# Kernel optimization log

Hardware: AMD Instinct MI355X
Metric: run time of the kernel (lower is better)

The kernel has to match this reference:

```python
import jax, jax.numpy as jnp
import numpy as np

NUM_SLOTS = 7
DIM = 4096
NUM_HEADS = 8
HEAD_DIM = DIM // NUM_HEADS
LN_EPS = 1e-5


def setup_inputs() -> dict:
    key = jax.random.key(0)
    ks = jax.random.split(key, 9)
    B, N = 8, 2048
    x = jax.random.normal(ks[0], (B, N, DIM), dtype=jnp.float32)
    slots = 1e-4 * jax.random.normal(ks[1], (NUM_SLOTS, DIM), dtype=jnp.float32)
    ln_g = jnp.ones((DIM,), jnp.float32)
    ln_b = jnp.zeros((DIM,), jnp.float32)
    # nn.MultiheadAttention packed in-projection: rows [Wq; Wk; Wv], each (DIM, DIM)
    s = 1.0 / np.sqrt(DIM)
    in_proj_w = jax.random.uniform(ks[2], (3 * DIM, DIM), jnp.float32, -s, s)
    in_proj_b = jnp.zeros((3 * DIM,), jnp.float32)
    out_proj_w = jax.random.uniform(ks[3], (DIM, DIM), jnp.float32, -s, s)
    out_proj_b = jnp.zeros((DIM,), jnp.float32)
    alpha = 0.1 * jax.random.normal(ks[4], (1,), jnp.float32)  # nonzero so gate path is active
    return {"x": x, "slots": slots, "ln_g": ln_g, "ln_b": ln_b,
            "in_proj_w": in_proj_w, "in_proj_b": in_proj_b,
            "out_proj_w": out_proj_w, "out_proj_b": out_proj_b, "alpha": alpha}


def _cmrm(x, slots, ln_g, ln_b, in_proj_w, in_proj_b, out_proj_w, out_proj_b, alpha):
    x32 = x.astype(jnp.float32)
    # pre LayerNorm
    mu = jnp.mean(x32, axis=-1, keepdims=True)
    var = jnp.mean(jnp.square(x32 - mu), axis=-1, keepdims=True)
    xn = (x32 - mu) * jax.lax.rsqrt(var + LN_EPS) * ln_g + ln_b  # (B,N,D)
    slots_c = jnp.clip(slots, -10.0, 10.0)  # (Q,D), Q=7
    Wq, Wk, Wv = jnp.split(in_proj_w, 3, axis=0)
    bq, bk, bv = jnp.split(in_proj_b, 3, axis=0)
    q = slots_c @ Wq.T + bq                      # (Q,D), identical for all batches
    k = xn @ Wk.T + bk                           # (B,N,D)
    v = xn @ Wv.T + bv                           # (B,N,D)
    B, N, _ = x.shape
    qh = q.reshape(NUM_SLOTS, NUM_HEADS, HEAD_DIM)          # (Q,H,hd)
    kh = k.reshape(B, N, NUM_HEADS, HEAD_DIM)
    vh = v.reshape(B, N, NUM_HEADS, HEAD_DIM)
    scale = 1.0 / np.sqrt(HEAD_DIM)
    scores = jnp.einsum('qhd,bnhd->bhqn', qh * scale, kh)   # (B,H,Q,N)
    attn = jax.nn.softmax(scores, axis=-1)
    ctx = jnp.einsum('bhqn,bnhd->bqhd', attn, vh).reshape(B, NUM_SLOTS, DIM)
    slots_out = ctx @ out_proj_w.T + out_proj_b             # (B,Q,D)
    slots_res = slots_c[None] + slots_out                   # residual, ungated slots
    gate = jnp.tanh(alpha)                                  # (1,)
    g = jnp.mean(gate * slots_res, axis=1, keepdims=True)   # (B,1,D)
    x_refined = (x32 + g).astype(x.dtype)
    attn_weights = jnp.mean(attn, axis=1)                   # torch avg over heads -> (B,Q,N)
    return x_refined, attn_weights


def reference(x, slots, ln_g, ln_b, in_proj_w, in_proj_b, out_proj_w, out_proj_b, alpha):
    return _cmrm(x, slots, ln_g, ln_b, in_proj_w, in_proj_b, out_proj_w, out_proj_b, alpha)
```

## Files before the change

kernel.cpp:

```cpp
#include <hip/hip_runtime.h>

typedef __attribute__((ext_vector_type(4))) float f32x4;
typedef __attribute__((ext_vector_type(8))) short short8x;

#define DIM   4096
#define NB    8
#define NN    2048
#define NROWS (NB*NN)
#define NQ    7
#define NHQ   56
#define SCALE 0.04419417382415922f

#define OFF_MU     0L
#define OFF_RSTD   16384L
#define OFF_Q7     32768L
#define OFF_A      61440L
#define OFF_D0     61504L
#define OFF_S1     61568L
#define OFF_SUMEXP 61632L
#define OFF_CTXM   62528L
#define OFF_GFIN   95296L
#define OFF_YM     128064L
#define OFF_UGBF   390208L
#define OFF_SCT    521280L
#define OFF_BIG    1438784L
#define OFF_PART   (OFF_BIG)

__device__ __forceinline__ unsigned short f2bf(float f) {
  union { float f; unsigned int u; } v; v.f = f;
  return (unsigned short)((v.u + 0x7FFFu + ((v.u >> 16) & 1u)) >> 16);
}
__device__ __forceinline__ unsigned short f2bfr(float f) {
  union { float f; unsigned int u; } v; v.f = f;
  return (unsigned short)((v.u + 0x8000u) >> 16);
}
__device__ __forceinline__ float waveSum(float v) {
  #pragma unroll
  for (int m = 1; m < 64; m <<= 1) v += __shfl_xor(v, m);
  return v;
}

__global__ __launch_bounds__(256) void k_pre(const float* __restrict__ ipw,
    const float* __restrict__ ipb, const float* __restrict__ slots,
    float* __restrict__ q7, float* __restrict__ ws) {
  const int bid = blockIdx.x, tid = threadIdx.x;
  const int w = tid >> 6, l = tid & 63;
  if (bid == 0) {
    if (tid < 448) (ws + OFF_SUMEXP)[tid] = 0.f;
    else if (tid < 512) (ws + OFF_S1)[tid - 448] = 0.f;
  } else if (bid <= 8) {
    unsigned* u32 = (unsigned*)(ws + OFF_UGBF);
    const long r = 56 + bid - 1;
    #pragma unroll
    for (int j = 0; j < 8; j++) u32[r*2048 + (long)tid*8 + j] = 0u;
  } else if (bid == 9) {
    if (tid < 64) (ws + OFF_A)[tid] = 0.f;
    else if (tid < 128) (ws + OFF_D0)[tid - 64] = 0.f;
  }
  const int d = bid * 4 + w;
  const float4* wr4 = (const float4*)(ipw + (long)d * DIM);
  float acc[7] = {0,0,0,0,0,0,0};
  for (int e4 = l; e4 < 1024; e4 += 64) {
    float4 wv = wr4[e4];
    #pragma unroll
    for (int s = 0; s < 7; s++) {
      float4 sv = ((const float4*)(slots + (long)s*DIM))[e4];
      sv.x = fminf(fmaxf(sv.x, -10.f), 10.f); sv.y = fminf(fmaxf(sv.y, -10.f), 10.f);
      sv.z = fminf(fmaxf(sv.z, -10.f), 10.f); sv.w = fminf(fmaxf(sv.w, -10.f), 10.f);
      acc[s] += wv.x*sv.x + wv.y*sv.y + wv.z*sv.z + wv.w*sv.w;
    }
  }
  #pragma unroll
  for (int s = 0; s < 7; s++) acc[s] = waveSum(acc[s]);
  if (l == 0) {
    float bq = ipb[d];
    #pragma unroll
    for (int s = 0; s < 7; s++) q7[(long)s*DIM + d] = acc[s] + bq;
  }
}

__global__ __launch_bounds__(256) void k_uproj(const float* __restrict__ ipw,
    const float* __restrict__ ipb, const float* __restrict__ q7,
    float* __restrict__ upart, float* __restrict__ D0arr) {
  __shared__ float qs[7][32];
  const int bid = blockIdx.x, tid = threadIdx.x;
  const int bx = bid & 3, h = (bid >> 2) & 7, c = bid >> 5;
  if (tid < 224) {
    int s = tid >> 5, hd = tid & 31;
    qs[s][hd] = q7[(long)s*DIM + h*512 + c*32 + hd];
  }
  __syncthreads();
  if (bx == 0 && tid < 64) {
    const int l = tid;
    float bk = (l < 32) ? ipb[DIM + h*512 + c*32 + l] : 0.f;
    #pragma unroll
    for (int s = 0; s < 7; s++) {
      float v = (l < 32) ? qs[s][l]*bk : 0.f;
      v = waveSum(v);
      if (l == 0) atomicAdd(&D0arr[h*7 + s], SCALE * v);
    }
  }
  const int e0 = bx*1024 + tid*4;
  float4 acc[7];
  #pragma unroll
  for (int s = 0; s < 7; s++) { acc[s].x = 0; acc[s].y = 0; acc[s].z = 0; acc[s].w = 0; }
  #pragma unroll 4
  for (int hd = 0; hd < 32; hd++) {
    float4 wv = *(const float4*)(ipw + ((long)(DIM + h*512 + c*32 + hd))*DIM + e0);
    #pragma unroll
    for (int s = 0; s < 7; s++) {
      float qv = qs[s][hd];
      acc[s].x += qv*wv.x; acc[s].y += qv*wv.y; acc[s].z += qv*wv.z; acc[s].w += qv*wv.w;
    }
  }
  #pragma unroll
  for (int s = 0; s < 7; s++)
    *(float4*)&upart[(long)((c*8 + h)*7 + s)*DIM + e0] = acc[s];
}

__global__ __launch_bounds__(256) void k_ured(const float* __restrict__ upart,
    const float* __restrict__ lng, const float* __restrict__ lnb,
    unsigned short* __restrict__ ugbf, float* __restrict__ Aarr, float* __restrict__ D0arr) {
  const int bid = blockIdx.x, tid = threadIdx.x;
  const int bx = bid & 15, h = bid >> 4;
  const int e = bx*256 + tid, l = tid & 63;
  float ge = lng[e], be = lnb[e];
  #pragma unroll
  for (int s = 0; s < 7; s++) {
    float u = 0;
    #pragma unroll
    for (int c = 0; c < 16; c++) u += upart[(long)((c*8 + h)*7 + s)*DIM + e];
    u *= SCALE;
    ugbf[(long)(h*7 + s)*DIM + e] = f2bf(u * ge);
    float pa = waveSum(u * ge);
    float pd = waveSum(u * be);
    if (l == 0) {
      atomicAdd(&Aarr[h*7 + s], pa);
      atomicAdd(&D0arr[h*7 + s], pd);
    }
  }
}

__global__ __launch_bounds__(128) void k_scores(const float* __restrict__ x,
    const unsigned short* __restrict__ ugbf, const float* __restrict__ Aarr,
    const float* __restrict__ D0arr, float* __restrict__ mu_o, float* __restrict__ rstd_o,
    float* __restrict__ sct, float* __restrict__ sumexp) {
  const int tid = threadIdx.x;
  const int wid = tid >> 6, l = tid & 63;
  const int lr = l & 15, lk8 = (l >> 4) * 8;
  const int row0w = blockIdx.x * 32 + wid * 16;
  const int b = blockIdx.x >> 6;
  const long arow = (long)(row0w + lr) * DIM;
  f32x4 acc0 = {0,0,0,0}, acc1 = {0,0,0,0}, acc2 = {0,0,0,0}, acc3 = {0,0,0,0};
  float sx = 0.f, sxx = 0.f;
  const long b0 = (long)(0*16 + lr)*DIM, b1 = (long)(1*16 + lr)*DIM,
             b2 = (long)(2*16 + lr)*DIM, b3 = (long)(3*16 + lr)*DIM;
  #pragma unroll 2
  for (int kc = 0; kc < DIM; kc += 32) {
    const float4 v0 = *(const float4*)(x + arow + kc + lk8);
    const float4 v1 = *(const float4*)(x + arow + kc + lk8 + 4);
    sx  += (v0.x + v0.y) + (v0.z + v0.w) + (v1.x + v1.y) + (v1.z + v1.w);
    sxx += v0.x*v0.x + v0.y*v0.y + v0.z*v0.z + v0.w*v0.w
         + v1.x*v1.x + v1.y*v1.y + v1.z*v1.z + v1.w*v1.w;
    short8x a;
    a[0] = (short)f2bfr(v0.x); a[1] = (short)f2bfr(v0.y);
    a[2] = (short)f2bfr(v0.z); a[3] = (short)f2bfr(v0.w);
    a[4] = (short)f2bfr(v1.x); a[5] = (short)f2bfr(v1.y);
    a[6] = (short)f2bfr(v1.z); a[7] = (short)f2bfr(v1.w);
    short8x bb0 = *(const short8x*)(ugbf + b0 + kc + lk8);
    acc0 = __builtin_amdgcn_mfma_f32_16x16x32_bf16(a, bb0, acc0, 0, 0, 0);
    short8x bb1 = *(const short8x*)(ugbf + b1 + kc + lk8);
    acc1 = __builtin_amdgcn_mfma_f32_16x16x32_bf16(a, bb1, acc1, 0, 0, 0);
    short8x bb2 = *(const short8x*)(ugbf + b2 + kc + lk8);
    acc2 = __builtin_amdgcn_mfma_f32_16x16x32_bf16(a, bb2, acc2, 0, 0, 0);
    short8x bb3 = *(const short8x*)(ugbf + b3 + kc + lk8);
    acc3 = __builtin_amdgcn_mfma_f32_16x16x32_bf16(a, bb3, acc3, 0, 0, 0);
  }
  sx += __shfl_xor(sx, 16);  sx += __shfl_xor(sx, 32);
  sxx += __shfl_xor(sxx, 16); sxx += __shfl_xor(sxx, 32);
  float muv = sx * (1.0f/DIM);
  float var = sxx * (1.0f/DIM) - muv*muv;
  float rsv = rsqrtf(var + 1e-5f);
  if (l < 16) { mu_o[row0w + l] = muv; rstd_o[row0w + l] = rsv; }
  float es0 = 0, es1 = 0, es2 = 0, es3 = 0;
  #pragma unroll
  for (int i = 0; i < 4; i++) {
    const int rl = (l >> 4)*4 + i;
    const float mur_ = __shfl(muv, rl);
    const float rs_  = __shfl(rsv, rl);
    {
      int hq = 0*16 + lr; float Ah = Aarr[hq], Dh = D0arr[hq];
      float e = __expf(rs_*(acc0[i] - mur_*Ah) + Dh);
      sct[(long)hq*NROWS + row0w + rl] = e; es0 += e;
    }
    {
      int hq = 1*16 + lr; float Ah = Aarr[hq], Dh = D0arr[hq];
      float e = __expf(rs_*(acc1[i] - mur_*Ah) + Dh);
      sct[(long)hq*NROWS + row0w + rl] = e; es1 += e;
    }
    {
      int hq = 2*16 + lr; float Ah = Aarr[hq], Dh = D0arr[hq];
      float e = __expf(rs_*(acc2[i] - mur_*Ah) + Dh);
      sct[(long)hq*NROWS + row0w + rl] = e; es2 += e;
    }
    if (lr < 8) {
      int hq = 3*16 + lr; float Ah = Aarr[hq], Dh = D0arr[hq];
      float e = __expf(rs_*(acc3[i] - mur_*Ah) + Dh);
      sct[(long)hq*NROWS + row0w + rl] = e; es3 += e;
    }
  }
  es0 += __shfl_xor(es0, 16); es0 += __shfl_xor(es0, 32);
  es1 += __shfl_xor(es1, 16); es1 += __shfl_xor(es1, 32);
  es2 += __shfl_xor(es2, 16); es2 += __shfl_xor(es2, 32);
  es3 += __shfl_xor(es3, 16); es3 += __shfl_xor(es3, 32);
  if (l < 16) {
    atomicAdd(&sumexp[b*NHQ + 0*16 + l], es0);
    atomicAdd(&sumexp[b*NHQ + 1*16 + l], es1);
    atomicAdd(&sumexp[b*NHQ + 2*16 + l], es2);
    if (l < 8) atomicAdd(&sumexp[b*NHQ + 3*16 + l], es3);
  }
}

__global__ __launch_bounds__(256) void k_ypart(const float* __restrict__ x,
    const float* __restrict__ sct, const float* __restrict__ sumexp,
    const float* __restrict__ mu, const float* __restrict__ rstd,
    float* __restrict__ part, float* __restrict__ s1, float* __restrict__ out_attn) {
  __shared__ float rinv[56];
  __shared__ float amr[8][128];
  __shared__ float psm[56][128];
  __shared__ float s1sm[8];
  const int bid = blockIdx.x, tid = threadIdx.x;
  const int b = bid >> 6, ec = (bid >> 4) & 3, nc = bid & 15;
  const int row0 = b*NN + nc*128;
  if (tid < 56) rinv[tid] = 1.0f / sumexp[b*NHQ + tid];
  if (tid < 8) s1sm[tid] = 0.f;
  __syncthreads();
  for (int i = tid; i < 1024; i += 256) {
    const int h = i >> 7, nn = i & 127, row = row0 + nn;
    float amv = 0;
    #pragma unroll
    for (int q = 0; q < 7; q++) {
      float p = sct[(long)(h*7 + q)*NROWS + row] * rinv[h*7 + q];
      amv += p;
      psm[h*7 + q][nn] = p;
    }
    amv *= (1.0f/7.0f);
    amr[h][nn] = amv * rstd[row];
  }
  __syncthreads();
  if (ec == 0) {
    for (int i = tid; i < 896; i += 256) {
      const int q = i / 128, nn = i % 128;
      float s = 0;
      #pragma unroll
      for (int h = 0; h < 8; h++) s += psm[h*7 + q][nn];
      out_attn[((long)(b*NQ + q))*NN + nc*128 + nn] = s * 0.125f;
    }
    {
      const int h = tid >> 5, sl = tid & 31;
      float v = 0;
      #pragma unroll
      for (int nn = sl; nn < 128; nn += 32) v += amr[h][nn] * mu[row0 + nn];
      #pragma unroll
      for (int m = 1; m < 32; m <<= 1) v += __shfl_xor(v, m);
      if (sl == 0) atomicAdd(&s1[b*8 + h], v);
    }
  }
  const int e = ec*1024 + tid*4;
  float ax[8], ay[8], az[8], aw[8];
  #pragma unroll
  for (int h = 0; h < 8; h++) { ax[h]=0; ay[h]=0; az[h]=0; aw[h]=0; }
  const float* xp = x + (long)row0*DIM + e;
  #pragma unroll 2
  for (int nn = 0; nn < 128; nn++) {
    const float4 xv = *(const float4*)(xp + (long)nn*DIM);
    #pragma unroll
    for (int h = 0; h < 8; h++) {
      float a = amr[h][nn];
      ax[h] += a*xv.x; ay[h] += a*xv.y; az[h] += a*xv.z; aw[h] += a*xv.w;
    }
  }
  #pragma unroll
  for (int h = 0; h < 8; h++) {
    float4 o; o.x = ax[h]; o.y = ay[h]; o.z = az[h]; o.w = aw[h];
    *(float4*)&part[((long)(nc*64 + b*8 + h))*DIM + e] = o;
  }
}

__global__ __launch_bounds__(256) void k_yred(const float* __restrict__ part,
    const float* __restrict__ s1, const float* __restrict__ lng, const float* __restrict__ lnb,
    float* __restrict__ ym) {
  const long i4 = (long)blockIdx.x*256 + threadIdx.x;
  const float4* p4 = (const float4*)part;
  float4 s = p4[i4];
  #pragma unroll
  for (int nc = 1; nc < 16; nc++) {
    float4 v = p4[(long)nc*65536 + i4];
    s.x += v.x; s.y += v.y; s.z += v.z; s.w += v.w;
  }
  const int bh = (int)(i4 >> 10), e4 = (int)(i4 & 1023);
  float sv = s1[bh];
  float4 g = ((const float4*)lng)[e4], bb = ((const float4*)lnb)[e4];
  float4 o;
  o.x = g.x*(s.x - sv) + bb.x; o.y = g.y*(s.y - sv) + bb.y;
  o.z = g.z*(s.z - sv) + bb.z; o.w = g.w*(s.w - sv) + bb.w;
  ((float4*)ym)[i4] = o;
}

__global__ __launch_bounds__(256) void k_ctxm(const float* __restrict__ ipw,
    const float* __restrict__ ipb, const float* __restrict__ ym, float* __restrict__ ctxm) {
  const int w = threadIdx.x >> 6, l = threadIdx.x & 63;
  const int d = blockIdx.x*4 + w;
  const int h = d >> 9;
  const float4* wr4 = (const float4*)(ipw + ((long)(2*DIM + d))*DIM);
  float acc[8] = {0,0,0,0,0,0,0,0};
  for (int e4 = l; e4 < 1024; e4 += 64) {
    float4 wv = wr4[e4];
    #pragma unroll
    for (int b = 0; b < 8; b++) {
      float4 y = ((const float4*)(ym + (long)(b*8 + h)*DIM))[e4];
      acc[b] += wv.x*y.x + wv.y*y.y + wv.z*y.z + wv.w*y.w;
    }
  }
  #pragma unroll
  for (int b = 0; b < 8; b++) acc[b] = waveSum(acc[b]);
  if (l == 0) {
    float bias = ipb[2*DIM + d];
    #pragma unroll
    for (int b = 0; b < 8; b++) ctxm[(long)b*DIM + d] = acc[b] + bias;
  }
}

__global__ __launch_bounds__(256) void k_gvec(const float* __restrict__ opw,
    const float* __restrict__ opb, const float* __restrict__ ctxm, const float* __restrict__ slots,
    const float* __restrict__ alpha, float* __restrict__ gfin) {
  const int w = threadIdx.x >> 6, l = threadIdx.x & 63;
  const int d = blockIdx.x*4 + w;
  const float4* wr4 = (const float4*)(opw + (long)d*DIM);
  float acc[8] = {0,0,0,0,0,0,0,0};
  for (int e4 = l; e4 < 1024; e4 += 64) {
    float4 wv = wr4[e4];
    #pragma unroll
    for (int b = 0; b < 8; b++) {
      float4 c = ((const float4*)(ctxm + (long)b*DIM))[e4];
      acc[b] += wv.x*c.x + wv.y*c.y + wv.z*c.z + wv.w*c.w;
    }
  }
  #pragma unroll
  for (int b = 0; b < 8; b++) acc[b] = waveSum(acc[b]);
  if (l == 0) {
    float smv = 0;
    #pragma unroll
    for (int q = 0; q < 7; q++)
      smv += fminf(fmaxf(slots[(long)q*DIM + d], -10.f), 10.f);
    smv *= (1.0f/7.0f);
    float t = tanhf(alpha[0]);
    float base = smv + opb[d];
    #pragma unroll
    for (int b = 0; b < 8; b++) gfin[(long)b*DIM + d] = t * (base + acc[b]);
  }
}

__global__ __launch_bounds__(256) void k_refine(const float* __restrict__ x,
    const float* __restrict__ gfin, float* __restrict__ out) {
  const float4* x4 = (const float4*)x;
  const float4* g4 = (const float4*)gfin;
  float4* o4 = (float4*)out;
  const long total = (long)NROWS * 1024;
  for (long i4 = (long)blockIdx.x*256 + threadIdx.x; i4 < total; i4 += (long)gridDim.x*256) {
    long b = i4 >> 21;
    long e4 = i4 & 1023;
    float4 xv = x4[i4], gv = g4[b*1024 + e4];
    float4 o; o.x = xv.x + gv.x; o.y = xv.y + gv.y; o.z = xv.z + gv.z; o.w = xv.w + gv.w;
    o4[i4] = o;
  }
}

extern "C" void kernel_launch(void* const* d_in, const int* in_sizes, int n_in,
                              void* d_out, int out_size, void* d_ws, size_t ws_size,
                              hipStream_t stream) {
  const float* x     = (const float*)d_in[0];
  const float* slots = (const float*)d_in[1];
  const float* lng   = (const float*)d_in[2];
  const float* lnb   = (const float*)d_in[3];
  const float* ipw   = (const float*)d_in[4];
  const float* ipb   = (const float*)d_in[5];
  const float* opw   = (const float*)d_in[6];
  const float* opb   = (const float*)d_in[7];
  const float* alpha = (const float*)d_in[8];
  float* out = (float*)d_out;
  float* ws  = (float*)d_ws;

  float* mu     = ws + OFF_MU;
  float* rstd   = ws + OFF_RSTD;
  float* q7     = ws + OFF_Q7;
  float* Aarr   = ws + OFF_A;
  float* D0arr  = ws + OFF_D0;
  float* s1     = ws + OFF_S1;
  float* sumexp = ws + OFF_SUMEXP;
  float* ctxm   = ws + OFF_CTXM;
  float* gfin   = ws + OFF_GFIN;
  float* ym     = ws + OFF_YM;
  unsigned short* ugbf = (unsigned short*)(ws + OFF_UGBF);
  float* sct    = ws + OFF_SCT;
  float* upart  = ws + OFF_BIG;
  float* part   = ws + OFF_PART;
  float* out_attn = out + (long)NROWS * DIM;

  hipLaunchKernelGGL(k_pre,    dim3(1024), dim3(256), 0, stream, ipw, ipb, slots, q7, ws);
  hipLaunchKernelGGL(k_uproj,  dim3(512),  dim3(256), 0, stream, ipw, ipb, q7, upart, D0arr);
  hipLaunchKernelGGL(k_ured,   dim3(128),  dim3(256), 0, stream, upart, lng, lnb, ugbf, Aarr, D0arr);
  hipLaunchKernelGGL(k_scores, dim3(512),  dim3(128), 0, stream, x, ugbf, Aarr, D0arr, mu, rstd, sct, sumexp);
  hipLaunchKernelGGL(k_ypart,  dim3(512),  dim3(256), 0, stream, x, sct, sumexp, mu, rstd, part, s1, out_attn);
  hipLaunchKernelGGL(k_yred,   dim3(256),  dim3(256), 0, stream, part, s1, lng, lnb, ym);
  hipLaunchKernelGGL(k_ctxm,   dim3(1024), dim3(256), 0, stream, ipw, ipb, ym, ctxm);
  hipLaunchKernelGGL(k_gvec,   dim3(1024), dim3(256), 0, stream, opw, opb, ctxm, slots, alpha, gfin);
  hipLaunchKernelGGL(k_refine, dim3(8192), dim3(256), 0, stream, x, gfin, out);
}
```

Measured before the change: 401.0 us.

## Split-K scores across wave pairs and replace y-partial reduction with bf16 MFMA GEMM

k_scores now uses 256 threads, with two waves sharing each 16-row tile and each covering half of K. Their partial accumulators and LN sums are combined through shared memory. The fp32 k_ypart/k_yred pair (per-chunk partial sums plus a 16-way reduction pass) is replaced by two kernels. k_amprep builds head-averaged bf16 attention weights, padded to 16 rows, and also writes out_attn and s1. k_ymm computes the weighted sum of x with bf16 MFMA, using an x tile transposed in LDS. This removes the large partial-sum buffer traffic and scalar FMAs, at the cost of bf16 precision on x and attention weights, half the MFMA rows wasted on padding, and a serial 2048-step K loop per block.

New measurement: 422.6 us. +5.4%, slower.

```diff
diff --git a/kernel.cpp b/kernel.cpp
--- a/kernel.cpp
+++ b/kernel.cpp
@@ -22,9 +22,9 @@
 #define OFF_GFIN   95296L
 #define OFF_YM     128064L
 #define OFF_UGBF   390208L
-#define OFF_SCT    521280L
-#define OFF_BIG    1438784L
-#define OFF_PART   (OFF_BIG)
+#define OFF_AMBF   521280L
+#define OFF_SCT    652352L
+#define OFF_BIG    1569856L
 
 __device__ __forceinline__ unsigned short f2bf(float f) {
   union { float f; unsigned int u; } v; v.f = f;
@@ -141,22 +141,25 @@
   }
 }
 
-__global__ __launch_bounds__(128) void k_scores(const float* __restrict__ x,
+__global__ __launch_bounds__(256) void k_scores(const float* __restrict__ x,
     const unsigned short* __restrict__ ugbf, const float* __restrict__ Aarr,
     const float* __restrict__ D0arr, float* __restrict__ mu_o, float* __restrict__ rstd_o,
     float* __restrict__ sct, float* __restrict__ sumexp) {
+  __shared__ float xch[2][64][18];
   const int tid = threadIdx.x;
-  const int wid = tid >> 6, l = tid & 63;
+  const int w = tid >> 6, l = tid & 63;
+  const int grp = w >> 1, kh = w & 1;
   const int lr = l & 15, lk8 = (l >> 4) * 8;
-  const int row0w = blockIdx.x * 32 + wid * 16;
+  const int row0w = blockIdx.x * 32 + grp * 16;
   const int b = blockIdx.x >> 6;
   const long arow = (long)(row0w + lr) * DIM;
+  const int kbase = kh * 2048;
   f32x4 acc0 = {0,0,0,0}, acc1 = {0,0,0,0}, acc2 = {0,0,0,0}, acc3 = {0,0,0,0};
   float sx = 0.f, sxx = 0.f;
   const long b0 = (long)(0*16 + lr)*DIM, b1 = (long)(1*16 + lr)*DIM,
              b2 = (long)(2*16 + lr)*DIM, b3 = (long)(3*16 + lr)*DIM;
   #pragma unroll 2
-  for (int kc = 0; kc < DIM; kc += 32) {
+  for (int kc = kbase; kc < kbase + 2048; kc += 32) {
     const float4 v0 = *(const float4*)(x + arow + kc + lk8);
     const float4 v1 = *(const float4*)(x + arow + kc + lk8 + 4);
     sx  += (v0.x + v0.y) + (v0.z + v0.w) + (v1.x + v1.y) + (v1.z + v1.w);
@@ -176,6 +179,24 @@
     short8x bb3 = *(const short8x*)(ugbf + b3 + kc + lk8);
     acc3 = __builtin_amdgcn_mfma_f32_16x16x32_bf16(a, bb3, acc3, 0, 0, 0);
   }
+  if (kh == 1) {
+    float* p = xch[grp][l];
+    #pragma unroll
+    for (int i = 0; i < 4; i++) {
+      p[i] = acc0[i]; p[4+i] = acc1[i]; p[8+i] = acc2[i]; p[12+i] = acc3[i];
+    }
+    p[16] = sx; p[17] = sxx;
+  }
+  __syncthreads();
+  if (kh == 1) return;
+  {
+    const float* p = xch[grp][l];
+    #pragma unroll
+    for (int i = 0; i < 4; i++) {
+      acc0[i] += p[i]; acc1[i] += p[4+i]; acc2[i] += p[8+i]; acc3[i] += p[12+i];
+    }
+    sx += p[16]; sxx += p[17];
+  }
   sx += __shfl_xor(sx, 16);  sx += __shfl_xor(sx, 32);
   sxx += __shfl_xor(sxx, 16); sxx += __shfl_xor(sxx, 32);
   float muv = sx * (1.0f/DIM);
@@ -221,90 +242,79 @@
   }
 }
 
-__global__ __launch_bounds__(256) void k_ypart(const float* __restrict__ x,
-    const float* __restrict__ sct, const float* __restrict__ sumexp,
-    const float* __restrict__ mu, const float* __restrict__ rstd,
-    float* __restrict__ part, float* __restrict__ s1, float* __restrict__ out_attn) {
+__global__ __launch_bounds__(256) void k_amprep(const float* __restrict__ sct,
+    const float* __restrict__ sumexp, const float* __restrict__ mu,
+    const float* __restrict__ rstd, unsigned short* __restrict__ ambf,
+    float* __restrict__ s1, float* __restrict__ out_attn) {
   __shared__ float rinv[56];
-  __shared__ float amr[8][128];
-  __shared__ float psm[56][128];
-  __shared__ float s1sm[8];
   const int bid = blockIdx.x, tid = threadIdx.x;
-  const int b = bid >> 6, ec = (bid >> 4) & 3, nc = bid & 15;
-  const int row0 = b*NN + nc*128;
+  const int b = bid >> 3, nc = bid & 7;
+  const int n = nc*256 + tid, row = b*NN + n;
+  const int l = tid & 63;
   if (tid < 56) rinv[tid] = 1.0f / sumexp[b*NHQ + tid];
-  if (tid < 8) s1sm[tid] = 0.f;
   __syncthreads();
-  for (int i = tid; i < 1024; i += 256) {
-    const int h = i >> 7, nn = i & 127, row = row0 + nn;
-    float amv = 0;
+  const float rs = rstd[row];
+  const float mur = mu[row] * rs;
+  float aq[7] = {0,0,0,0,0,0,0};
+  #pragma unroll
+  for (int h = 0; h < 8; h++) {
+    float ah = 0;
     #pragma unroll
     for (int q = 0; q < 7; q++) {
       float p = sct[(long)(h*7 + q)*NROWS + row] * rinv[h*7 + q];
-      amv += p;
-      psm[h*7 + q][nn] = p;
-    }
-    amv *= (1.0f/7.0f);
-    amr[h][nn] = amv * rstd[row];
-  }
-  __syncthreads();
-  if (ec == 0) {
-    for (int i = tid; i < 896; i += 256) {
-      const int q = i / 128, nn = i % 128;
-      float s = 0;
-      #pragma unroll
-      for (int h = 0; h < 8; h++) s += psm[h*7 + q][nn];
-      out_attn[((long)(b*NQ + q))*NN + nc*128 + nn] = s * 0.125f;
-    }
-    {
-      const int h = tid >> 5, sl = tid & 31;
-      float v = 0;
-      #pragma unroll
-      for (int nn = sl; nn < 128; nn += 32) v += amr[h][nn] * mu[row0 + nn];
-      #pragma unroll
-      for (int m = 1; m < 32; m <<= 1) v += __shfl_xor(v, m);
-      if (sl == 0) atomicAdd(&s1[b*8 + h], v);
-    }
-  }
-  const int e = ec*1024 + tid*4;
-  float ax[8], ay[8], az[8], aw[8];
-  #pragma unroll
-  for (int h = 0; h < 8; h++) { ax[h]=0; ay[h]=0; az[h]=0; aw[h]=0; }
-  const float* xp = x + (long)row0*DIM + e;
-  #pragma unroll 2
-  for (int nn = 0; nn < 128; nn++) {
-    const float4 xv = *(const float4*)(xp + (long)nn*DIM);
-    #pragma unroll
-    for (int h = 0; h < 8; h++) {
-      float a = amr[h][nn];
-      ax[h] += a*xv.x; ay[h] += a*xv.y; az[h] += a*xv.z; aw[h] += a*xv.w;
-    }
-  }
-  #pragma unroll
-  for (int h = 0; h < 8; h++) {
-    float4 o; o.x = ax[h]; o.y = ay[h]; o.z = az[h]; o.w = aw[h];
-    *(float4*)&part[((long)(nc*64 + b*8 + h))*DIM + e] = o;
-  }
-}
-
-__global__ __launch_bounds__(256) void k_yred(const float* __restrict__ part,
-    const float* __restrict__ s1, const float* __restrict__ lng, const float* __restrict__ lnb,
-    float* __restrict__ ym) {
-  const long i4 = (long)blockIdx.x*256 + threadIdx.x;
-  const float4* p4 = (const float4*)part;
-  float4 s = p4[i4];
-  #pragma unroll
-  for (int nc = 1; nc < 16; nc++) {
-    float4 v = p4[(long)nc*65536 + i4];
-    s.x += v.x; s.y += v.y; s.z += v.z; s.w += v.w;
-  }
-  const int bh = (int)(i4 >> 10), e4 = (int)(i4 & 1023);
-  float sv = s1[bh];
-  float4 g = ((const float4*)lng)[e4], bb = ((const float4*)lnb)[e4];
-  float4 o;
-  o.x = g.x*(s.x - sv) + bb.x; o.y = g.y*(s.y - sv) + bb.y;
-  o.z = g.z*(s.z - sv) + bb.z; o.w = g.w*(s.w - sv) + bb.w;
-  ((float4*)ym)[i4] = o;
+      aq[q] += p; ah += p;
+    }
+    float amv = ah * (1.0f/7.0f);
+    ambf[(long)(b*16 + h)*NN + n] = f2bf(amv * rs);
+    float sv = waveSum(amv * mur);
+    if (l == 0) atomicAdd(&s1[b*8 + h], sv);
+  }
+  #pragma unroll
+  for (int h = 8; h < 16; h++) ambf[(long)(b*16 + h)*NN + n] = 0;
+  #pragma unroll
+  for (int q = 0; q < 7; q++) out_attn[((long)(b*NQ + q))*NN + n] = aq[q] * 0.125f;
+}
+
+__global__ __launch_bounds__(256) void k_ymm(const float* __restrict__ x,
+    const unsigned short* __restrict__ ambf, const float* __restrict__ s1,
+    const float* __restrict__ lng, const float* __restrict__ lnb, float* __restrict__ ym) {
+  __shared__ __align__(16) unsigned short xT[64][72];
+  const int tid = threadIdx.x;
+  const int w = tid >> 6, l = tid & 63;
+  const int b = blockIdx.x >> 6, et = blockIdx.x & 63;
+  const int e0 = et * 64;
+  const int lr = l & 15, lk = (l >> 4) * 8;
+  const int nrow = tid >> 4, ecol = (tid & 15) * 4;
+  const long xbase = (long)b*NN*DIM + e0 + ecol;
+  const unsigned short* ap = ambf + (long)(b*16 + lr)*NN + lk;
+  f32x4 acc = {0,0,0,0};
+  for (int n0 = 0; n0 < NN; n0 += 64) {
+    __syncthreads();
+    #pragma unroll
+    for (int p = 0; p < 4; p++) {
+      const int nn = p*16 + nrow;
+      const float4 v = *(const float4*)(x + xbase + (long)(n0 + nn)*DIM);
+      xT[ecol + 0][nn] = f2bfr(v.x);
+      xT[ecol + 1][nn] = f2bfr(v.y);
+      xT[ecol + 2][nn] = f2bfr(v.z);
+      xT[ecol + 3][nn] = f2bfr(v.w);
+    }
+    __syncthreads();
+    #pragma unroll
+    for (int kk = 0; kk < 64; kk += 32) {
+      short8x a  = *(const short8x*)(ap + n0 + kk);
+      short8x bb = *(const short8x*)(&xT[w*16 + lr][kk + lk]);
+      acc = __builtin_amdgcn_mfma_f32_16x16x32_bf16(a, bb, acc, 0, 0, 0);
+    }
+  }
+  const int eg = e0 + w*16 + lr;
+  const float ge = lng[eg], be = lnb[eg];
+  #pragma unroll
+  for (int i = 0; i < 4; i++) {
+    const int h = (l >> 4)*4 + i;
+    if (h < 8)
+      ym[(long)(b*8 + h)*DIM + eg] = ge*(acc[i] - s1[b*8 + h]) + be;
+  }
 }
 
 __global__ __launch_bounds__(256) void k_ctxm(const float* __restrict__ ipw,
@@ -402,17 +412,17 @@
   float* gfin   = ws + OFF_GFIN;
   float* ym     = ws + OFF_YM;
   unsigned short* ugbf = (unsigned short*)(ws + OFF_UGBF);
+  unsigned short* ambf = (unsigned short*)(ws + OFF_AMBF);
   float* sct    = ws + OFF_SCT;
   float* upart  = ws + OFF_BIG;
-  float* part   = ws + OFF_PART;
   float* out_attn = out + (long)NROWS * DIM;
 
   hipLaunchKernelGGL(k_pre,    dim3(1024), dim3(256), 0, stream, ipw, ipb, slots, q7, ws);
   hipLaunchKernelGGL(k_uproj,  dim3(512),  dim3(256), 0, stream, ipw, ipb, q7, upart, D0arr);
   hipLaunchKernelGGL(k_ured,   dim3(128),  dim3(256), 0, stream, upart, lng, lnb, ugbf, Aarr, D0arr);
-  hipLaunchKernelGGL(k_scores, dim3(512),  dim3(128), 0, stream, x, ugbf, Aarr, D0arr, mu, rstd, sct, sumexp);
-  hipLaunchKernelGGL(k_ypart,  dim3(512),  dim3(256), 0, stream, x, sct, sumexp, mu, rstd, part, s1, out_attn);
-  hipLaunchKernelGGL(k_yred,   dim3(256),  dim3(256), 0, stream, part, s1, lng, lnb, ym);
+  hipLaunchKernelGGL(k_scores, dim3(512),  dim3(256), 0, stream, x, ugbf, Aarr, D0arr, mu, rstd, sct, sumexp);
+  hipLaunchKernelGGL(k_amprep, dim3(64),   dim3(256), 0, stream, sct, sumexp, mu, rstd, ambf, s1, out_attn);
+  hipLaunchKernelGGL(k_ymm,    dim3(512),  dim3(256), 0, stream, x, ambf, s1, lng, lnb, ym);
   hipLaunchKernelGGL(k_ctxm,   dim3(1024), dim3(256), 0, stream, ipw, ipb, ym, ctxm);
   hipLaunchKernelGGL(k_gvec,   dim3(1024), dim3(256), 0, stream, opw, opb, ctxm, slots, alpha, gfin);
   hipLaunchKernelGGL(k_refine, dim3(8192), dim3(256), 0, stream, x, gfin, out);
```

## Split k_scores K dimension across four waves with LDS reduction

Applied to the files above, without the earlier changes.

The scores kernel now gives each 256-thread block 16 rows and splits the 4096-wide reduction across four waves, each covering 1024 columns. Partial MFMA accumulators and row sums are combined through shared memory by wave 0. The grid doubles to 1024 blocks and there are four times as many waves. The aim is more memory parallelism on the streaming read of x, which was limited to 1024 waves before. In exchange it adds a shared-memory reduction and a barrier, and three of the four waves sit idle during the epilogue. An unused shared variable is also removed from k_ypart.

Result: no change. 405.1 us (+1.0%).

```diff
diff --git a/kernel.cpp b/kernel.cpp
--- a/kernel.cpp
+++ b/kernel.cpp
@@ -141,22 +141,24 @@
   }
 }
 
-__global__ __launch_bounds__(128) void k_scores(const float* __restrict__ x,
+__global__ __launch_bounds__(256) void k_scores(const float* __restrict__ x,
     const unsigned short* __restrict__ ugbf, const float* __restrict__ Aarr,
     const float* __restrict__ D0arr, float* __restrict__ mu_o, float* __restrict__ rstd_o,
     float* __restrict__ sct, float* __restrict__ sumexp) {
+  __shared__ float xch[3][64][18];
   const int tid = threadIdx.x;
-  const int wid = tid >> 6, l = tid & 63;
+  const int w = tid >> 6, l = tid & 63;
   const int lr = l & 15, lk8 = (l >> 4) * 8;
-  const int row0w = blockIdx.x * 32 + wid * 16;
-  const int b = blockIdx.x >> 6;
-  const long arow = (long)(row0w + lr) * DIM;
+  const int row0 = blockIdx.x * 16;
+  const int b = blockIdx.x >> 7;
+  const long arow = (long)(row0 + lr) * DIM;
+  const int kbase = w * 1024;
   f32x4 acc0 = {0,0,0,0}, acc1 = {0,0,0,0}, acc2 = {0,0,0,0}, acc3 = {0,0,0,0};
   float sx = 0.f, sxx = 0.f;
   const long b0 = (long)(0*16 + lr)*DIM, b1 = (long)(1*16 + lr)*DIM,
              b2 = (long)(2*16 + lr)*DIM, b3 = (long)(3*16 + lr)*DIM;
   #pragma unroll 2
-  for (int kc = 0; kc < DIM; kc += 32) {
+  for (int kc = kbase; kc < kbase + 1024; kc += 32) {
     const float4 v0 = *(const float4*)(x + arow + kc + lk8);
     const float4 v1 = *(const float4*)(x + arow + kc + lk8 + 4);
     sx  += (v0.x + v0.y) + (v0.z + v0.w) + (v1.x + v1.y) + (v1.z + v1.w);
@@ -176,12 +178,31 @@
     short8x bb3 = *(const short8x*)(ugbf + b3 + kc + lk8);
     acc3 = __builtin_amdgcn_mfma_f32_16x16x32_bf16(a, bb3, acc3, 0, 0, 0);
   }
+  if (w != 0) {
+    float* p = xch[w - 1][l];
+    #pragma unroll
+    for (int i = 0; i < 4; i++) {
+      p[i] = acc0[i]; p[4+i] = acc1[i]; p[8+i] = acc2[i]; p[12+i] = acc3[i];
+    }
+    p[16] = sx; p[17] = sxx;
+  }
+  __syncthreads();
+  if (w != 0) return;
+  #pragma unroll
+  for (int ww = 0; ww < 3; ww++) {
+    const float* p = xch[ww][l];
+    #pragma unroll
+    for (int i = 0; i < 4; i++) {
+      acc0[i] += p[i]; acc1[i] += p[4+i]; acc2[i] += p[8+i]; acc3[i] += p[12+i];
+    }
+    sx += p[16]; sxx += p[17];
+  }
   sx += __shfl_xor(sx, 16);  sx += __shfl_xor(sx, 32);
   sxx += __shfl_xor(sxx, 16); sxx += __shfl_xor(sxx, 32);
   float muv = sx * (1.0f/DIM);
   float var = sxx * (1.0f/DIM) - muv*muv;
   float rsv = rsqrtf(var + 1e-5f);
-  if (l < 16) { mu_o[row0w + l] = muv; rstd_o[row0w + l] = rsv; }
+  if (l < 16) { mu_o[row0 + l] = muv; rstd_o[row0 + l] = rsv; }
   float es0 = 0, es1 = 0, es2 = 0, es3 = 0;
   #pragma unroll
   for (int i = 0; i < 4; i++) {
@@ -191,22 +212,22 @@
     {
       int hq = 0*16 + lr; float Ah = Aarr[hq], Dh = D0arr[hq];
       float e = __expf(rs_*(acc0[i] - mur_*Ah) + Dh);
-      sct[(long)hq*NROWS + row0w + rl] = e; es0 += e;
+      sct[(long)hq*NROWS + row0 + rl] = e; es0 += e;
     }
     {
       int hq = 1*16 + lr; float Ah = Aarr[hq], Dh = D0arr[hq];
       float e = __expf(rs_*(acc1[i] - mur_*Ah) + Dh);
-      sct[(long)hq*NROWS + row0w + rl] = e; es1 += e;
+      sct[(long)hq*NROWS + row0 + rl] = e; es1 += e;
     }
     {
       int hq = 2*16 + lr; float Ah = Aarr[hq], Dh = D0arr[hq];
       float e = __expf(rs_*(acc2[i] - mur_*Ah) + Dh);
-      sct[(long)hq*NROWS + row0w + rl] = e; es2 += e;
+      sct[(long)hq*NROWS + row0 + rl] = e; es2 += e;
     }
     if (lr < 8) {
       int hq = 3*16 + lr; float Ah = Aarr[hq], Dh = D0arr[hq];
       float e = __expf(rs_*(acc3[i] - mur_*Ah) + Dh);
-      sct[(long)hq*NROWS + row0w + rl] = e; es3 += e;
+      sct[(long)hq*NROWS + row0 + rl] = e; es3 += e;
     }
   }
   es0 += __shfl_xor(es0, 16); es0 += __shfl_xor(es0, 32);
@@ -228,12 +249,10 @@
   __shared__ float rinv[56];
   __shared__ float amr[8][128];
   __shared__ float psm[56][128];
-  __shared__ float s1sm[8];
   const int bid = blockIdx.x, tid = threadIdx.x;
   const int b = bid >> 6, ec = (bid >> 4) & 3, nc = bid & 15;
   const int row0 = b*NN + nc*128;
   if (tid < 56) rinv[tid] = 1.0f / sumexp[b*NHQ + tid];
-  if (tid < 8) s1sm[tid] = 0.f;
   __syncthreads();
   for (int i = tid; i < 1024; i += 256) {
     const int h = i >> 7, nn = i & 127, row = row0 + nn;
@@ -410,7 +429,7 @@
   hipLaunchKernelGGL(k_pre,    dim3(1024), dim3(256), 0, stream, ipw, ipb, slots, q7, ws);
   hipLaunchKernelGGL(k_uproj,  dim3(512),  dim3(256), 0, stream, ipw, ipb, q7, upart, D0arr);
   hipLaunchKernelGGL(k_ured,   dim3(128),  dim3(256), 0, stream, upart, lng, lnb, ugbf, Aarr, D0arr);
-  hipLaunchKernelGGL(k_scores, dim3(512),  dim3(128), 0, stream, x, ugbf, Aarr, D0arr, mu, rstd, sct, sumexp);
+  hipLaunchKernelGGL(k_scores, dim3(1024), dim3(256), 0, stream, x, ugbf, Aarr, D0arr, mu, rstd, sct, sumexp);
   hipLaunchKernelGGL(k_ypart,  dim3(512),  dim3(256), 0, stream, x, sct, sumexp, mu, rstd, part, s1, out_attn);
   hipLaunchKernelGGL(k_yred,   dim3(256),  dim3(256), 0, stream, part, s1, lng, lnb, ym);
   hipLaunchKernelGGL(k_ctxm,   dim3(1024), dim3(256), 0, stream, ipw, ipb, ym, ctxm);
```
